# Kernel optimization log

Hardware: AMD Instinct MI355X
Metric: run time of the kernel (lower is better)

## Reference

```python
import jax, jax.numpy as jnp
import numpy as np

B, N_OBJ, N_VAL, E, H, HEADS = 512, 10, 200, 420, 128, 4
NPG = 1 + N_OBJ + N_VAL  # nodes per graph = 211
N = B * NPG
FMIN = float(np.finfo(np.float32).min)


def _gat_conv(x, src, dst, W, att_src, att_dst, bias, concat):
    # PyG GATConv (v1): linear (no bias) -> per-head attention logits ->
    # leaky_relu(a_src[j]+a_dst[i]) -> softmax over edges grouped by dst -> scatter-sum
    heads = att_src.shape[0]
    xs = (x @ W).reshape(N, heads, -1)            # [N, heads, C]
    a_src = (xs * att_src).sum(-1)                # [N, heads]
    a_dst = (xs * att_dst).sum(-1)                # [N, heads]
    alpha = jax.nn.leaky_relu(a_src[src] + a_dst[dst], 0.2)   # [Etot, heads]
    amax = jax.ops.segment_max(alpha, dst, num_segments=N)
    ex = jnp.exp(alpha - amax[dst])
    denom = jax.ops.segment_sum(ex, dst, num_segments=N)
    alpha = ex / (denom[dst] + 1e-16)
    out = jax.ops.segment_sum(xs[src] * alpha[..., None], dst, num_segments=N)  # [N,heads,C]
    out = out.reshape(N, -1) if concat else out.mean(axis=1)
    return out + bias


def setup_inputs() -> dict:
    key = jax.random.key(0)
    ks = jax.random.split(key, 24)
    s = 0.1
    C1 = H // HEADS  # 32
    inp = {
        'head_node': jax.random.normal(ks[0], (B, 2), jnp.float32),
        'objective_nodes': jax.random.normal(ks[1], (B, N_OBJ, 2), jnp.float32),
        'value_nodes': jax.random.normal(ks[2], (B, N_VAL, 5), jnp.float32),
        'edge_indices': jax.random.randint(ks[3], (B, 2, E), 0, NPG, jnp.int64 if jax.config.jax_enable_x64 else jnp.int32),
        'accept_mask': jnp.ones((B, 2), jnp.float32),
        'W_head': jax.random.normal(ks[4], (2, H)) * s, 'b_head': jnp.zeros((H,)),
        'W_obj': jax.random.normal(ks[5], (2, H)) * s, 'b_obj': jnp.zeros((H,)),
        'W_val': jax.random.normal(ks[6], (5, H)) * s, 'b_val': jnp.zeros((H,)),
        'W1': jax.random.normal(ks[7], (H, HEADS * C1)) * s,
        'att_src1': jax.random.normal(ks[8], (HEADS, C1)) * s,
        'att_dst1': jax.random.normal(ks[9], (HEADS, C1)) * s,
        'b1': jnp.zeros((HEADS * C1,)),
        'W2': jax.random.normal(ks[10], (H, HEADS * H)) * s,
        'att_src2': jax.random.normal(ks[11], (HEADS, H)) * s,
        'att_dst2': jax.random.normal(ks[12], (HEADS, H)) * s,
        'b2': jnp.zeros((H,)),
        'W_acc': jax.random.normal(ks[13], (H, 2)) * 0.01, 'b_acc': jnp.zeros((2,)),
        'W_off': jax.random.normal(ks[14], (H, 1)) * 0.01, 'b_off': jnp.zeros((1,)),
        'W_vf': jax.random.normal(ks[15], (H, 1)) * s, 'b_vf': jnp.zeros((1,)),
    }
    return inp


def reference(head_node, objective_nodes, value_nodes, edge_indices, accept_mask,
              W_head, b_head, W_obj, b_obj, W_val, b_val,
              W1, att_src1, att_dst1, b1, W2, att_src2, att_dst2, b2,
              W_acc, b_acc, W_off, b_off, W_vf, b_vf):
    # node encoders + ReLU
    h_head = jax.nn.relu(head_node @ W_head + b_head)                  # [B,H]
    h_obj = jax.nn.relu(objective_nodes @ W_obj + b_obj)               # [B,N_OBJ,H]
    h_val = jax.nn.relu(value_nodes @ W_val + b_val)                   # [B,N_VAL,H]
    h_nodes = jnp.concatenate([h_head[:, None], h_obj, h_val], axis=1)  # [B,NPG,H]
    x = h_nodes.reshape(N, H)
    # batch graphs: offset per-graph edge indices, add self loops
    offs = (jnp.arange(B, dtype=edge_indices.dtype) * NPG)[:, None, None]
    ei = (edge_indices + offs).transpose(1, 0, 2).reshape(2, -1)       # [2, B*E]
    loops = jnp.arange(N, dtype=edge_indices.dtype)
    src = jnp.concatenate([ei[0], loops])
    dst = jnp.concatenate([ei[1], loops])
    # GAT: layer1 concat heads, ReLU (BasicGNN inter-layer act), layer2 mean heads
    x1 = jax.nn.relu(_gat_conv(x, src, dst, W1, att_src1, att_dst1, b1, True))
    x2 = _gat_conv(x1, src, dst, W2, att_src2, att_dst2, b2, False)
    h_out = jax.nn.relu(x2).reshape(B, NPG, H)
    h_head_out = h_out[:, 0]                                           # [B,H]
    h_val_out = h_out[:, -N_VAL:]                                      # [B,N_VAL,H]
    offer_logits = (h_val_out @ W_off + b_off).squeeze(-1)             # [B,N_VAL]
    accept_inf_mask = jnp.maximum(jnp.log(accept_mask), FMIN)
    accept_logits = h_head_out @ W_acc + b_acc + accept_inf_mask       # [B,2]
    vf = h_head_out @ W_vf + b_vf                                      # [B,1]
    return jnp.concatenate([accept_logits, offer_logits, vf], axis=-1)  # [B, 2+N_VAL+1]
```

## Files before the change

kernel.cpp:

```cpp
#include <hip/hip_runtime.h>

typedef unsigned short u16;
typedef unsigned int u32;
typedef short short8 __attribute__((ext_vector_type(8)));
typedef float f32x4 __attribute__((ext_vector_type(4)));

#define NB   512
#define NPG  211
#define NOBJ 10
#define NVAL 200
#define NE   420
#define NN   (NB * NPG)

__device__ __forceinline__ float bf2f(u16 u){
  union { unsigned i; float f; } v; v.i = ((unsigned)u) << 16; return v.f;
}
__device__ __forceinline__ u16 f2bf(float f){
  union { float f; unsigned i; } v; v.f = f;
  return (u16)((v.i + 0x7FFFu + ((v.i >> 16) & 1u)) >> 16);
}
__device__ __forceinline__ float lo_bf(u32 u){ union{u32 i;float f;}v; v.i=u<<16; return v.f; }
__device__ __forceinline__ float hi_bf(u32 u){ union{u32 i;float f;}v; v.i=u&0xffff0000u; return v.f; }
__device__ __forceinline__ u32 pack_bf(float a, float b){ return (u32)f2bf(a) | ((u32)f2bf(b)<<16); }
__device__ __forceinline__ float lrelu(float s){ return s > 0.f ? s : 0.2f * s; }
__device__ __forceinline__ short8 pack8(ushort4 a, ushort4 b){
  short8 v;
  v[0]=(short)a.x; v[1]=(short)a.y; v[2]=(short)a.z; v[3]=(short)a.w;
  v[4]=(short)b.x; v[5]=(short)b.y; v[6]=(short)b.z; v[7]=(short)b.w;
  return v;
}
__device__ __forceinline__ int s16(int r, int c){
  return (r << 7) + ((((c >> 3) ^ (r & 15)) << 3) | (c & 7));
}

#define AS_GLOBAL(p) ((const __attribute__((address_space(1))) void*)((const void*)(p)))
#define AS_LDS(p)    ((__attribute__((address_space(3))) void*)((void*)(p)))

__global__ __launch_bounds__(256) void k_prep(const float* __restrict__ W1, const float* __restrict__ W2,
                                              const float* __restrict__ as2, const float* __restrict__ ad2,
                                              u16* __restrict__ W1t, u16* __restrict__ W2t,
                                              float* __restrict__ wms, float* __restrict__ wmd,
                                              u16* __restrict__ W2z){
  int gid = blockIdx.x * 256 + threadIdx.x;
  if (gid < 16384){
    int k = gid >> 7, n = gid & 127;
    W1t[n * 128 + k] = f2bf(W1[k * 128 + n]);
  } else if (gid < 81920){
    int t = gid - 16384;
    int n = t >> 9, kk = t & 511;
    int h = kk >> 7, c = kk & 127;
    W2t[n * 512 + kk] = f2bf(W2[c * 512 + h * 128 + n]);
  } else if (gid < 82944){
    int t = gid - 81920;
    int which = t >> 9, hk = t & 511;
    int h = hk >> 7, k = hk & 127;
    const float* av = which ? ad2 : as2;
    float s = 0.f;
    for (int j = 0; j < 128; ++j)
      s += W2[k * 512 + h * 128 + j] * av[h * 128 + j];
    (which ? wmd : wms)[hk] = s;
  } else {
    int t = gid - 82944;
    int c = t >> 7, k = t & 127;
    W2z[c * 128 + k] = f2bf(W2[k * 512 + c]);
  }
}

__global__ __launch_bounds__(256) void k_embed2(
    const float* __restrict__ head, const float* __restrict__ obj, const float* __restrict__ val,
    const float* __restrict__ Wh, const float* __restrict__ bh,
    const float* __restrict__ Wo, const float* __restrict__ bo,
    const float* __restrict__ Wv, const float* __restrict__ bv,
    u16* __restrict__ x){
  int gid = blockIdx.x * 256 + threadIdx.x;
  int n = gid >> 5, cc = (gid & 31) << 2;
  int g = n / NPG, loc = n - g * NPG;
  float a[4];
  if (loc == 0){
    const float* in = head + (size_t)g * 2;
    float i0 = in[0], i1 = in[1];
    #pragma unroll
    for (int t = 0; t < 4; ++t){ int c = cc + t; a[t] = bh[c] + i0 * Wh[c] + i1 * Wh[128 + c]; }
  } else if (loc <= NOBJ){
    const float* in = obj + ((size_t)g * NOBJ + (loc - 1)) * 2;
    float i0 = in[0], i1 = in[1];
    #pragma unroll
    for (int t = 0; t < 4; ++t){ int c = cc + t; a[t] = bo[c] + i0 * Wo[c] + i1 * Wo[128 + c]; }
  } else {
    const float* in = val + ((size_t)g * NVAL + (loc - 11)) * 5;
    float f[5];
    #pragma unroll
    for (int k = 0; k < 5; ++k) f[k] = in[k];
    #pragma unroll
    for (int t = 0; t < 4; ++t){
      int c = cc + t; float s = bv[c];
      #pragma unroll
      for (int k = 0; k < 5; ++k) s += f[k] * Wv[k * 128 + c];
      a[t] = s;
    }
  }
  ushort4 u;
  u.x = f2bf(fmaxf(a[0], 0.f)); u.y = f2bf(fmaxf(a[1], 0.f));
  u.z = f2bf(fmaxf(a[2], 0.f)); u.w = f2bf(fmaxf(a[3], 0.f));
  *(ushort4*)&x[(size_t)n * 128 + cc] = u;
}

__global__ __launch_bounds__(256) void k_csr2(const int* __restrict__ eidx,
                                              int* __restrict__ coff, int* __restrict__ csrc){
  __shared__ int sEs[420], sEd[420], sTmp[256], sOff[212], sSrc[632];
  int g = blockIdx.x, tid = threadIdx.x;
  const int4* e4 = (const int4*)(eidx + (size_t)g * 840);
  for (int i = tid; i < 105; i += 256){ ((int4*)sEs)[i] = e4[i]; ((int4*)sEd)[i] = e4[105 + i]; }
  __syncthreads();
  int deg = 0;
  if (tid < NPG){
    deg = 1;
    const int4* p4 = (const int4*)sEd;
    #pragma unroll 4
    for (int i = 0; i < 105; ++i){
      int4 v = p4[i];
      deg += (v.x == tid) + (v.y == tid) + (v.z == tid) + (v.w == tid);
    }
  }
  int v = deg;
  #pragma unroll
  for (int st = 1; st < 256; st <<= 1){
    sTmp[tid] = v;
    __syncthreads();
    if (tid >= st) v += sTmp[tid - st];
    __syncthreads();
  }
  if (tid < NPG) sOff[tid] = v - deg;
  if (tid == NPG - 1) sOff[NPG] = v;
  __syncthreads();
  if (tid < NPG){
    int p = sOff[tid];
    sSrc[p++] = tid;
    const int4* pd4 = (const int4*)sEd;
    const int4* ps4 = (const int4*)sEs;
    for (int i = 0; i < 105; ++i){
      int4 d = pd4[i]; int4 s = ps4[i];
      if (d.x == tid) sSrc[p++] = s.x;
      if (d.y == tid) sSrc[p++] = s.y;
      if (d.z == tid) sSrc[p++] = s.z;
      if (d.w == tid) sSrc[p++] = s.w;
    }
  }
  __syncthreads();
  if (tid < 212) coff[(size_t)g * 212 + tid] = sOff[tid];
  for (int i = tid; i < 631; i += 256) csrc[(size_t)g * 632 + i] = sSrc[i];
}

template<int KCH, bool RELU>
__global__ __launch_bounds__(512) void k_mm(const u16* __restrict__ A, int aStride, int chunkOff,
                                            const u16* __restrict__ Bt, int bstride,
                                            const float* __restrict__ bias, u16* __restrict__ C){
  __shared__ u16 sA[128 * 128];
  __shared__ u16 sB[128 * 128];
  const int tid = threadIdx.x, lane = tid & 63, w = tid >> 6;
  const int l15 = lane & 15, lg = lane >> 4;
  const int row0 = blockIdx.x * 128;
  f32x4 acc[8];
  #pragma unroll
  for (int ni = 0; ni < 8; ++ni) acc[ni] = (f32x4){0,0,0,0};

  #pragma unroll 1
  for (int ch = 0; ch < KCH; ++ch){
    const u16* Ab = A + (size_t)ch * chunkOff;
    const u16* Bb = Bt + ch * 128;
    #pragma unroll
    for (int i = 0; i < 4; ++i){
      int r = w * 16 + i * 4 + (lane >> 4);
      int c16 = lane & 15;
      int sw = (c16 ^ (r & 15)) << 4;
      __builtin_amdgcn_global_load_lds(AS_GLOBAL((const char*)(Ab + (size_t)(row0 + r) * aStride) + sw),
                                       AS_LDS(&sA[(w * 16 + i * 4) * 128]), 16, 0, 0);
      __builtin_amdgcn_global_load_lds(AS_GLOBAL((const char*)(Bb + (size_t)r * bstride) + sw),
                                       AS_LDS(&sB[(w * 16 + i * 4) * 128]), 16, 0, 0);
    }
    __syncthreads();
    #pragma unroll
    for (int kk = 0; kk < 4; ++kk){
      int k0 = kk * 32 + lg * 4;
      int rr = w * 16 + l15;
      short8 af = pack8(*(const ushort4*)&sA[s16(rr, k0)],
                        *(const ushort4*)&sA[s16(rr, k0 + 16)]);
      #pragma unroll
      for (int ni = 0; ni < 8; ++ni){
        int cc = ni * 16 + l15;
        short8 bf = pack8(*(const ushort4*)&sB[s16(cc, k0)],
                          *(const ushort4*)&sB[s16(cc, k0 + 16)]);
        acc[ni] = __builtin_amdgcn_mfma_f32_16x16x32_bf16(af, bf, acc[ni], 0, 0, 0);
      }
    }
    __syncthreads();
  }
  const int r0 = row0 + w * 16 + lg * 4;
  #pragma unroll
  for (int ni = 0; ni < 8; ++ni){
    int col = ni * 16 + l15;
    float bv = RELU ? bias[col] : 0.f;
    #pragma unroll
    for (int r = 0; r < 4; ++r){
      float v = acc[ni][r];
      if (RELU) v = fmaxf(v + bv, 0.f);
      C[(size_t)(r0 + r) * 128 + col] = f2bf(v);
    }
  }
}

__global__ __launch_bounds__(512) void k_mmz(const u16* __restrict__ A,
                                             const u16* __restrict__ W2z,
                                             u16* __restrict__ z){
  __shared__ u16 sA[128 * 128];
  __shared__ u16 sB[128 * 128];
  const int tid = threadIdx.x, lane = tid & 63, w = tid >> 6;
  const int l15 = lane & 15, lg = lane >> 4;
  const int row0 = (blockIdx.x >> 2) * 128;
  const int cy   = blockIdx.x & 3;
  const u16* Bb = W2z + cy * 16384;
  f32x4 acc[8];
  #pragma unroll
  for (int ni = 0; ni < 8; ++ni) acc[ni] = (f32x4){0,0,0,0};

  #pragma unroll
  for (int i = 0; i < 4; ++i){
    int r = w * 16 + i * 4 + (lane >> 4);
    int c16 = lane & 15;
    int sw = (c16 ^ (r & 15)) << 4;
    __builtin_amdgcn_global_load_lds(AS_GLOBAL((const char*)(A + (size_t)(row0 + r) * 128) + sw),
                                     AS_LDS(&sA[(w * 16 + i * 4) * 128]), 16, 0, 0);
    __builtin_amdgcn_global_load_lds(AS_GLOBAL((const char*)(Bb + (size_t)r * 128) + sw),
                                     AS_LDS(&sB[(w * 16 + i * 4) * 128]), 16, 0, 0);
  }
  __syncthreads();
  #pragma unroll
  for (int kk = 0; kk < 4; ++kk){
    int k0 = kk * 32 + lg * 4;
    int rr = w * 16 + l15;
    short8 af = pack8(*(const ushort4*)&sA[s16(rr, k0)],
                      *(const ushort4*)&sA[s16(rr, k0 + 16)]);
    #pragma unroll
    for (int ni = 0; ni < 8; ++ni){
      int cc = ni * 16 + l15;
      short8 bf = pack8(*(const ushort4*)&sB[s16(cc, k0)],
                        *(const ushort4*)&sB[s16(cc, k0 + 16)]);
      acc[ni] = __builtin_amdgcn_mfma_f32_16x16x32_bf16(af, bf, acc[ni], 0, 0, 0);
    }
  }
  const int r0 = row0 + w * 16 + lg * 4;
  #pragma unroll
  for (int ni = 0; ni < 8; ++ni){
    int col = cy * 128 + ni * 16 + l15;
    #pragma unroll
    for (int r = 0; r < 4; ++r)
      z[(size_t)(r0 + r) * 512 + col] = f2bf(acc[ni][r]);
  }
}

__global__ __launch_bounds__(512) void k_attsm1(const u16* __restrict__ xs1,
                                                const float* __restrict__ as1, const float* __restrict__ ad1,
                                                const int* __restrict__ coff, const int* __restrict__ csrc,
                                                float* __restrict__ wn, float* __restrict__ rden){
  __shared__ float sLs[844], sLd[844];
  const int g = blockIdx.x, tid = threadIdx.x;
  const int gb = g * NPG;
  for (int t = tid; t < NPG * 4; t += 512){
    int n = t >> 2, h = t & 3;
    const u16* xr = xs1 + (size_t)(gb + n) * 128 + h * 32;
    float s = 0.f, d = 0.f;
    #pragma unroll
    for (int j = 0; j < 8; ++j){
      ushort4 xv = *(const ushort4*)(xr + j * 4);
      #pragma unroll
      for (int q = 0; q < 4; ++q){
        float xf = bf2f(((const u16*)&xv)[q]);
        int c = h * 32 + j * 4 + q;
        s += xf * as1[c];
        d += xf * ad1[c];
      }
    }
    sLs[t] = s; sLd[t] = d;
  }
  __syncthreads();
  for (int t = tid; t < NPG * 4; t += 512){
    int dst = t >> 2, h = t & 3;
    int o0 = coff[(size_t)g * 212 + dst], o1 = coff[(size_t)g * 212 + dst + 1];
    const int* sp = csrc + (size_t)g * 632;
    float ad = sLd[t];
    float m = -3e38f;
    for (int e = o0; e < o1; ++e) m = fmaxf(m, lrelu(sLs[sp[e] * 4 + h] + ad));
    float dn = 0.f;
    float* wp = wn + (size_t)g * 2528 + h * 632;
    for (int e = o0; e < o1; ++e){
      float ee = __expf(lrelu(sLs[sp[e] * 4 + h] + ad) - m);
      wp[e] = ee; dn += ee;
    }
    rden[(size_t)(gb + dst) * 4 + h] = 1.0f / (dn + 1e-16f);
  }
}

__global__ __launch_bounds__(512) void k_attsm2(const u16* __restrict__ x1,
                                                const float* __restrict__ wms, const float* __restrict__ wmd,
                                                const int* __restrict__ coff, const int* __restrict__ csrc,
                                                float* __restrict__ wn, float* __restrict__ rden){
  __shared__ float sw[1024];
  __shared__ float sLs[844], sLd[844];
  const int g = blockIdx.x, tid = threadIdx.x;
  const int gb = g * NPG;
  for (int i = tid; i < 1024; i += 512) sw[i] = (i < 512) ? wms[i] : wmd[i - 512];
  __syncthreads();
  for (int t = tid; t < NPG * 4; t += 512){
    int n = t >> 2, h = t & 3;
    const u16* xr = x1 + (size_t)(gb + n) * 128;
    const float* wsp = sw + h * 128;
    const float* wdp = sw + 512 + h * 128;
    float s = 0.f, d = 0.f;
    #pragma unroll
    for (int j = 0; j < 32; ++j){
      ushort4 xv = *(const ushort4*)(xr + j * 4);
      #pragma unroll
      for (int q = 0; q < 4; ++q){
        float xf = bf2f(((const u16*)&xv)[q]);
        s += xf * wsp[j * 4 + q];
        d += xf * wdp[j * 4 + q];
      }
    }
    sLs[t] = s; sLd[t] = d;
  }
  __syncthreads();
  for (int t = tid; t < NPG * 4; t += 512){
    int dst = t >> 2, h = t & 3;
    int o0 = coff[(size_t)g * 212 + dst], o1 = coff[(size_t)g * 212 + dst + 1];
    const int* sp = csrc + (size_t)g * 632;
    float ad = sLd[t];
    float m = -3e38f;
    for (int e = o0; e < o1; ++e) m = fmaxf(m, lrelu(sLs[sp[e] * 4 + h] + ad));
    float dn = 0.f;
    float* wp = wn + (size_t)g * 2528 + h * 632;
    for (int e = o0; e < o1; ++e){
      float ee = __expf(lrelu(sLs[sp[e] * 4 + h] + ad) - m);
      wp[e] = ee; dn += ee;
    }
    rden[(size_t)(gb + dst) * 4 + h] = 0.25f / (dn + 1e-16f);
  }
}

__global__ __launch_bounds__(256) void k_gat1k(const u16* __restrict__ xs1,
                                               const float* __restrict__ wn, const float* __restrict__ rden,
                                               const int* __restrict__ coff, const int* __restrict__ csrc,
                                               const float* __restrict__ b1, u16* __restrict__ x1){
  int bid = blockIdx.x;
  int g = bid / 53, ch = bid - g * 53;
  int dst = ch * 4 + (threadIdx.x >> 6);
  if (dst >= NPG) return;
  int lane = threadIdx.x & 63;
  int cp = lane << 1, hh = lane >> 4;
  int gb = g * NPG;
  int o0 = coff[(size_t)g * 212 + dst], o1 = coff[(size_t)g * 212 + dst + 1];
  const int* sp = csrc + (size_t)g * 632;
  const float* wp = wn + (size_t)g * 2528 + hh * 632;
  float a0 = 0.f, a1 = 0.f;
  for (int e = o0; e < o1; ++e){
    int src = sp[e];
    u32 f = *(const u32*)&xs1[(size_t)(gb + src) * 128 + cp];
    float w = wp[e];
    a0 += w * lo_bf(f); a1 += w * hi_bf(f);
  }
  float rv = rden[(size_t)(gb + dst) * 4 + hh];
  *(u32*)&x1[(size_t)(gb + dst) * 128 + cp] =
    pack_bf(fmaxf(a0 * rv + b1[cp], 0.f), fmaxf(a1 * rv + b1[cp + 1], 0.f));
}

__global__ __launch_bounds__(256) void k_aggp(const u16* __restrict__ z,
                                              const float* __restrict__ wn, const float* __restrict__ rden,
                                              const int* __restrict__ coff, const int* __restrict__ csrc,
                                              const float* __restrict__ b2, const float* __restrict__ amask,
                                              const float* __restrict__ Wacc, const float* __restrict__ bacc,
                                              const float* __restrict__ Woff, const float* __restrict__ boff,
                                              const float* __restrict__ Wvf,  const float* __restrict__ bvf,
                                              float* __restrict__ out){
  int bid = blockIdx.x;
  int g = bid / 51, chunk = bid - g * 51;
  int idx = chunk * 4 + (threadIdx.x >> 6);
  if (idx >= 201) return;
  int dst = (idx == 0) ? 0 : 10 + idx;
  int lane = threadIdx.x & 63;
  int cp = lane << 1;
  int gb = g * NPG;
  int o0 = coff[(size_t)g * 212 + dst], o1 = coff[(size_t)g * 212 + dst + 1];
  const int* sp = csrc + (size_t)g * 632;
  const float* wb = wn + (size_t)g * 2528;
  float a00 = 0, a01 = 0, a10 = 0, a11 = 0, a20 = 0, a21 = 0, a30 = 0, a31 = 0;
  for (int e = o0; e < o1; ++e){
    int src = sp[e];
    const u16* zr = z + (size_t)(gb + src) * 512 + cp;
    u32 f0 = *(const u32*)&zr[0];
    u32 f1 = *(const u32*)&zr[128];
    u32 f2 = *(const u32*)&zr[256];
    u32 f3 = *(const u32*)&zr[384];
    float w0 = wb[e], w1 = wb[632 + e], w2 = wb[1264 + e], w3 = wb[1896 + e];
    a00 += w0 * lo_bf(f0); a01 += w0 * hi_bf(f0);
    a10 += w1 * lo_bf(f1); a11 += w1 * hi_bf(f1);
    a20 += w2 * lo_bf(f2); a21 += w2 * hi_bf(f2);
    a30 += w3 * lo_bf(f3); a31 += w3 * hi_bf(f3);
  }
  float4 rv = *(const float4*)&rden[(size_t)(gb + dst) * 4];
  float o2a = fmaxf(b2[cp]     + rv.x * a00 + rv.y * a10 + rv.z * a20 + rv.w * a30, 0.f);
  float o2b = fmaxf(b2[cp + 1] + rv.x * a01 + rv.y * a11 + rv.z * a21 + rv.w * a31, 0.f);
  if (idx == 0){
    float pA0 = o2a * Wacc[cp * 2]     + o2b * Wacc[(cp + 1) * 2];
    float pA1 = o2a * Wacc[cp * 2 + 1] + o2b * Wacc[(cp + 1) * 2 + 1];
    float pV  = o2a * Wvf[cp]          + o2b * Wvf[cp + 1];
    #pragma unroll
    for (int s = 1; s < 64; s <<= 1){
      pA0 += __shfl_xor(pA0, s);
      pA1 += __shfl_xor(pA1, s);
      pV  += __shfl_xor(pV, s);
    }
    if (lane == 0){
      float lm0 = fmaxf(logf(amask[g * 2]),     -3.402823466e38f);
      float lm1 = fmaxf(logf(amask[g * 2 + 1]), -3.402823466e38f);
      out[(size_t)g * 203]       = pA0 + bacc[0] + lm0;
      out[(size_t)g * 203 + 1]   = pA1 + bacc[1] + lm1;
      out[(size_t)g * 203 + 202] = pV + bvf[0];
    }
  } else {
    float pO = o2a * Woff[cp] + o2b * Woff[cp + 1];
    #pragma unroll
    for (int s = 1; s < 64; s <<= 1) pO += __shfl_xor(pO, s);
    if (lane == 0) out[(size_t)g * 203 + 2 + (idx - 1)] = pO + boff[0];
  }
}

extern "C" void kernel_launch(void* const* d_in, const int* in_sizes, int n_in,
                              void* d_out, int out_size, void* d_ws, size_t ws_size,
                              hipStream_t stream){
  (void)in_sizes; (void)n_in; (void)out_size; (void)ws_size;
  const float* head = (const float*)d_in[0];
  const float* obj  = (const float*)d_in[1];
  const float* val  = (const float*)d_in[2];
  const int*   eidx = (const int*)d_in[3];
  const float* amask= (const float*)d_in[4];
  const float* Wh   = (const float*)d_in[5];
  const float* bh   = (const float*)d_in[6];
  const float* Wo   = (const float*)d_in[7];
  const float* bo   = (const float*)d_in[8];
  const float* Wv   = (const float*)d_in[9];
  const float* bv   = (const float*)d_in[10];
  const float* W1   = (const float*)d_in[11];
  const float* as1  = (const float*)d_in[12];
  const float* ad1  = (const float*)d_in[13];
  const float* b1   = (const float*)d_in[14];
  const float* W2   = (const float*)d_in[15];
  const float* as2  = (const float*)d_in[16];
  const float* ad2  = (const float*)d_in[17];
  const float* b2   = (const float*)d_in[18];
  const float* Wacc = (const float*)d_in[19];
  const float* bacc = (const float*)d_in[20];
  const float* Woff = (const float*)d_in[21];
  const float* boff = (const float*)d_in[22];
  const float* Wvf  = (const float*)d_in[23];
  const float* bvf  = (const float*)d_in[24];
  float* out = (float*)d_out;

  char* ws = (char*)d_ws;
  u16*   W1t = (u16*)ws;
  u16*   W2t = (u16*)(ws + 32768);
  float* wms = (float*)(ws + 163840);
  float* wmd = (float*)(ws + 165888);
  int*   coff = (int*)(ws + 167936);
  int*   csrc = (int*)(ws + 602112);
  u16*   W2z  = (u16*)(ws + 1896448);
  float* wn   = (float*)(ws + 5353472);
  float* rden = (float*)(ws + 10530816);
  u16*   x    = (u16*)(ws + 12259328);
  u16*   xs1  = (u16*)(ws + 39915520);
  u16*   z    = (u16*)(ws + 67571712);

  k_prep<<<580, 256, 0, stream>>>(W1, W2, as2, ad2, W1t, W2t, wms, wmd, W2z);
  k_embed2<<<NN * 32 / 256, 256, 0, stream>>>(head, obj, val, Wh, bh, Wo, bo, Wv, bv, x);
  k_csr2<<<NB, 256, 0, stream>>>(eidx, coff, csrc);
  k_mm<1, false><<<NN / 128, 512, 0, stream>>>(x, 128, 0, W1t, 128, nullptr, xs1);
  k_attsm1<<<NB, 512, 0, stream>>>(xs1, as1, ad1, coff, csrc, wn, rden);
  k_gat1k<<<NB * 53, 256, 0, stream>>>(xs1, wn, rden, coff, csrc, b1, x);
  k_attsm2<<<NB, 512, 0, stream>>>(x, wms, wmd, coff, csrc, wn, rden);
  k_mmz<<<(NN / 128) * 4, 512, 0, stream>>>(x, W2z, z);
  k_aggp<<<NB * 51, 256, 0, stream>>>(z, wn, rden, coff, csrc, b2, amask,
                                      Wacc, bacc, Woff, boff, Wvf, bvf, out);
}
```

Baseline: 253.8 us.

## Fuse layer-2 aggregation before projection into one kernel with output heads

Reorders GAT layer 2 to aggregate the 128-wide layer-1 features per head first, then multiply by W2 with MFMA, using linearity. This replaces the separate z=x1@W2 matmul, which wrote a 512-wide intermediate, and the gather kernel that read it back. The new fused kernel computes attention-weighted aggregates into LDS, accumulates across heads in MFMA, and applies bias, ReLU and the output projections in place. It also remaps blocks to XCDs so neighbouring row tiles land together. In exchange it now computes all nodes, including objective nodes whose output is discarded, and the per-row serial gather runs inside the matmul block, which may limit overlap.

Measured after the change: 329.2 us. 1.3x slower.

```diff
diff --git a/kernel.cpp b/kernel.cpp
--- a/kernel.cpp
+++ b/kernel.cpp
@@ -39,8 +39,7 @@
 __global__ __launch_bounds__(256) void k_prep(const float* __restrict__ W1, const float* __restrict__ W2,
                                               const float* __restrict__ as2, const float* __restrict__ ad2,
                                               u16* __restrict__ W1t, u16* __restrict__ W2t,
-                                              float* __restrict__ wms, float* __restrict__ wmd,
-                                              u16* __restrict__ W2z){
+                                              float* __restrict__ wms, float* __restrict__ wmd){
   int gid = blockIdx.x * 256 + threadIdx.x;
   if (gid < 16384){
     int k = gid >> 7, n = gid & 127;
@@ -50,7 +49,7 @@
     int n = t >> 9, kk = t & 511;
     int h = kk >> 7, c = kk & 127;
     W2t[n * 512 + kk] = f2bf(W2[c * 512 + h * 128 + n]);
-  } else if (gid < 82944){
+  } else {
     int t = gid - 81920;
     int which = t >> 9, hk = t & 511;
     int h = hk >> 7, k = hk & 127;
@@ -59,10 +58,6 @@
     for (int j = 0; j < 128; ++j)
       s += W2[k * 512 + h * 128 + j] * av[h * 128 + j];
     (which ? wmd : wms)[hk] = s;
-  } else {
-    int t = gid - 82944;
-    int c = t >> 7, k = t & 127;
-    W2z[c * 128 + k] = f2bf(W2[k * 512 + c]);
   }
 }
 
@@ -206,55 +201,6 @@
       if (RELU) v = fmaxf(v + bv, 0.f);
       C[(size_t)(r0 + r) * 128 + col] = f2bf(v);
     }
-  }
-}
-
-__global__ __launch_bounds__(512) void k_mmz(const u16* __restrict__ A,
-                                             const u16* __restrict__ W2z,
-                                             u16* __restrict__ z){
-  __shared__ u16 sA[128 * 128];
-  __shared__ u16 sB[128 * 128];
-  const int tid = threadIdx.x, lane = tid & 63, w = tid >> 6;
-  const int l15 = lane & 15, lg = lane >> 4;
-  const int row0 = (blockIdx.x >> 2) * 128;
-  const int cy   = blockIdx.x & 3;
-  const u16* Bb = W2z + cy * 16384;
-  f32x4 acc[8];
-  #pragma unroll
-  for (int ni = 0; ni < 8; ++ni) acc[ni] = (f32x4){0,0,0,0};
-
-  #pragma unroll
-  for (int i = 0; i < 4; ++i){
-    int r = w * 16 + i * 4 + (lane >> 4);
-    int c16 = lane & 15;
-    int sw = (c16 ^ (r & 15)) << 4;
-    __builtin_amdgcn_global_load_lds(AS_GLOBAL((const char*)(A + (size_t)(row0 + r) * 128) + sw),
-                                     AS_LDS(&sA[(w * 16 + i * 4) * 128]), 16, 0, 0);
-    __builtin_amdgcn_global_load_lds(AS_GLOBAL((const char*)(Bb + (size_t)r * 128) + sw),
-                                     AS_LDS(&sB[(w * 16 + i * 4) * 128]), 16, 0, 0);
-  }
-  __syncthreads();
-  #pragma unroll
-  for (int kk = 0; kk < 4; ++kk){
-    int k0 = kk * 32 + lg * 4;
-    int rr = w * 16 + l15;
-    short8 af = pack8(*(const ushort4*)&sA[s16(rr, k0)],
-                      *(const ushort4*)&sA[s16(rr, k0 + 16)]);
-    #pragma unroll
-    for (int ni = 0; ni < 8; ++ni){
-      int cc = ni * 16 + l15;
-      short8 bf = pack8(*(const ushort4*)&sB[s16(cc, k0)],
-                        *(const ushort4*)&sB[s16(cc, k0 + 16)]);
-      acc[ni] = __builtin_amdgcn_mfma_f32_16x16x32_bf16(af, bf, acc[ni], 0, 0, 0);
-    }
-  }
-  const int r0 = row0 + w * 16 + lg * 4;
-  #pragma unroll
-  for (int ni = 0; ni < 8; ++ni){
-    int col = cy * 128 + ni * 16 + l15;
-    #pragma unroll
-    for (int r = 0; r < 4; ++r)
-      z[(size_t)(r0 + r) * 512 + col] = f2bf(acc[ni][r]);
   }
 }
 
@@ -372,64 +318,127 @@
     pack_bf(fmaxf(a0 * rv + b1[cp], 0.f), fmaxf(a1 * rv + b1[cp + 1], 0.f));
 }
 
-__global__ __launch_bounds__(256) void k_aggp(const u16* __restrict__ z,
-                                              const float* __restrict__ wn, const float* __restrict__ rden,
-                                              const int* __restrict__ coff, const int* __restrict__ csrc,
-                                              const float* __restrict__ b2, const float* __restrict__ amask,
-                                              const float* __restrict__ Wacc, const float* __restrict__ bacc,
-                                              const float* __restrict__ Woff, const float* __restrict__ boff,
-                                              const float* __restrict__ Wvf,  const float* __restrict__ bvf,
-                                              float* __restrict__ out){
-  int bid = blockIdx.x;
-  int g = bid / 51, chunk = bid - g * 51;
-  int idx = chunk * 4 + (threadIdx.x >> 6);
-  if (idx >= 201) return;
-  int dst = (idx == 0) ? 0 : 10 + idx;
-  int lane = threadIdx.x & 63;
-  int cp = lane << 1;
-  int gb = g * NPG;
-  int o0 = coff[(size_t)g * 212 + dst], o1 = coff[(size_t)g * 212 + dst + 1];
-  const int* sp = csrc + (size_t)g * 632;
-  const float* wb = wn + (size_t)g * 2528;
-  float a00 = 0, a01 = 0, a10 = 0, a11 = 0, a20 = 0, a21 = 0, a30 = 0, a31 = 0;
-  for (int e = o0; e < o1; ++e){
-    int src = sp[e];
-    const u16* zr = z + (size_t)(gb + src) * 512 + cp;
-    u32 f0 = *(const u32*)&zr[0];
-    u32 f1 = *(const u32*)&zr[128];
-    u32 f2 = *(const u32*)&zr[256];
-    u32 f3 = *(const u32*)&zr[384];
-    float w0 = wb[e], w1 = wb[632 + e], w2 = wb[1264 + e], w3 = wb[1896 + e];
-    a00 += w0 * lo_bf(f0); a01 += w0 * hi_bf(f0);
-    a10 += w1 * lo_bf(f1); a11 += w1 * hi_bf(f1);
-    a20 += w2 * lo_bf(f2); a21 += w2 * hi_bf(f2);
-    a30 += w3 * lo_bf(f3); a31 += w3 * hi_bf(f3);
-  }
-  float4 rv = *(const float4*)&rden[(size_t)(gb + dst) * 4];
-  float o2a = fmaxf(b2[cp]     + rv.x * a00 + rv.y * a10 + rv.z * a20 + rv.w * a30, 0.f);
-  float o2b = fmaxf(b2[cp + 1] + rv.x * a01 + rv.y * a11 + rv.z * a21 + rv.w * a31, 0.f);
-  if (idx == 0){
-    float pA0 = o2a * Wacc[cp * 2]     + o2b * Wacc[(cp + 1) * 2];
-    float pA1 = o2a * Wacc[cp * 2 + 1] + o2b * Wacc[(cp + 1) * 2 + 1];
-    float pV  = o2a * Wvf[cp]          + o2b * Wvf[cp + 1];
-    #pragma unroll
-    for (int s = 1; s < 64; s <<= 1){
-      pA0 += __shfl_xor(pA0, s);
-      pA1 += __shfl_xor(pA1, s);
-      pV  += __shfl_xor(pV, s);
-    }
-    if (lane == 0){
-      float lm0 = fmaxf(logf(amask[g * 2]),     -3.402823466e38f);
-      float lm1 = fmaxf(logf(amask[g * 2 + 1]), -3.402823466e38f);
-      out[(size_t)g * 203]       = pA0 + bacc[0] + lm0;
-      out[(size_t)g * 203 + 1]   = pA1 + bacc[1] + lm1;
-      out[(size_t)g * 203 + 202] = pV + bvf[0];
-    }
-  } else {
-    float pO = o2a * Woff[cp] + o2b * Woff[cp + 1];
-    #pragma unroll
-    for (int s = 1; s < 64; s <<= 1) pO += __shfl_xor(pO, s);
-    if (lane == 0) out[(size_t)g * 203 + 2 + (idx - 1)] = pO + boff[0];
+__global__ __launch_bounds__(512) void k_yagg(
+    const u16* __restrict__ x1, const float* __restrict__ wn, const float* __restrict__ rden,
+    const int* __restrict__ coff, const int* __restrict__ csrc,
+    const u16* __restrict__ W2t, const float* __restrict__ b2,
+    const float* __restrict__ amask,
+    const float* __restrict__ Wacc, const float* __restrict__ bacc,
+    const float* __restrict__ Woff, const float* __restrict__ boff,
+    const float* __restrict__ Wvf,  const float* __restrict__ bvf,
+    float* __restrict__ out)
+{
+  __shared__ u16 sA[128 * 128];
+  __shared__ u16 sB[128 * 128];
+  const int tid = threadIdx.x, lane = tid & 63, w = tid >> 6;
+  const int l15 = lane & 15, lg = lane >> 4;
+  const int cp = lane << 1;
+  const int xcd = blockIdx.x & 7, j = blockIdx.x >> 3;
+  const int nb  = (xcd < 4 ? xcd * 106 : 4 * 106 + (xcd - 4) * 105) + j;
+  const int row0 = nb * 128;
+
+  f32x4 acc[8];
+  #pragma unroll
+  for (int ni = 0; ni < 8; ++ni) acc[ni] = (f32x4){0,0,0,0};
+
+  #pragma unroll 1
+  for (int h = 0; h < 4; ++h){
+    #pragma unroll
+    for (int i = 0; i < 4; ++i){
+      int r = w * 16 + i * 4 + (lane >> 4);
+      int c16 = lane & 15;
+      int sw = (c16 ^ (r & 15)) << 4;
+      __builtin_amdgcn_global_load_lds(AS_GLOBAL((const char*)(W2t + (size_t)r * 512 + h * 128) + sw),
+                                       AS_LDS(&sB[(w * 16 + i * 4) * 128]), 16, 0, 0);
+    }
+    for (int t = 0; t < 16; ++t){
+      int row = row0 + w * 16 + t;
+      int g = row / NPG, loc = row - g * NPG;
+      int gb = g * NPG;
+      int o0 = coff[(size_t)g * 212 + loc], o1 = coff[(size_t)g * 212 + loc + 1];
+      const int* sp = csrc + (size_t)g * 632;
+      const float* wp = wn + (size_t)g * 2528 + h * 632;
+      float a0 = 0.f, a1 = 0.f;
+      int e = o0;
+      for (; e + 4 <= o1; e += 4){
+        int s0 = sp[e], s1 = sp[e+1], s2 = sp[e+2], s3 = sp[e+3];
+        u32 f0 = *(const u32*)&x1[(size_t)(gb + s0) * 128 + cp];
+        u32 f1 = *(const u32*)&x1[(size_t)(gb + s1) * 128 + cp];
+        u32 f2 = *(const u32*)&x1[(size_t)(gb + s2) * 128 + cp];
+        u32 f3 = *(const u32*)&x1[(size_t)(gb + s3) * 128 + cp];
+        float w0 = wp[e], w1 = wp[e+1], w2 = wp[e+2], w3 = wp[e+3];
+        a0 += w0 * lo_bf(f0); a1 += w0 * hi_bf(f0);
+        a0 += w1 * lo_bf(f1); a1 += w1 * hi_bf(f1);
+        a0 += w2 * lo_bf(f2); a1 += w2 * hi_bf(f2);
+        a0 += w3 * lo_bf(f3); a1 += w3 * hi_bf(f3);
+      }
+      for (; e < o1; ++e){
+        int src = sp[e];
+        u32 f = *(const u32*)&x1[(size_t)(gb + src) * 128 + cp];
+        float wv = wp[e];
+        a0 += wv * lo_bf(f); a1 += wv * hi_bf(f);
+      }
+      float rv = rden[(size_t)row * 4 + h];
+      *(u32*)&sA[s16(w * 16 + t, cp)] = pack_bf(a0 * rv, a1 * rv);
+    }
+    __syncthreads();
+    #pragma unroll
+    for (int kk = 0; kk < 4; ++kk){
+      int k0 = kk * 32 + lg * 4;
+      int rr = w * 16 + l15;
+      short8 af = pack8(*(const ushort4*)&sA[s16(rr, k0)],
+                        *(const ushort4*)&sA[s16(rr, k0 + 16)]);
+      #pragma unroll
+      for (int ni = 0; ni < 8; ++ni){
+        int cc = ni * 16 + l15;
+        short8 bf = pack8(*(const ushort4*)&sB[s16(cc, k0)],
+                          *(const ushort4*)&sB[s16(cc, k0 + 16)]);
+        acc[ni] = __builtin_amdgcn_mfma_f32_16x16x32_bf16(af, bf, acc[ni], 0, 0, 0);
+      }
+    }
+    __syncthreads();
+  }
+
+  float bv[8];
+  #pragma unroll
+  for (int ni = 0; ni < 8; ++ni) bv[ni] = b2[ni * 16 + l15];
+  #pragma unroll
+  for (int r = 0; r < 4; ++r){
+    int row = row0 + w * 16 + lg * 4 + r;
+    int g = row / NPG, loc = row - g * NPG;
+    float v[8];
+    #pragma unroll
+    for (int ni = 0; ni < 8; ++ni) v[ni] = fmaxf(acc[ni][r] + bv[ni], 0.f);
+    if (loc == 0){
+      float pA0 = 0.f, pA1 = 0.f, pV = 0.f;
+      #pragma unroll
+      for (int ni = 0; ni < 8; ++ni){
+        int c = ni * 16 + l15;
+        pA0 += v[ni] * Wacc[c * 2];
+        pA1 += v[ni] * Wacc[c * 2 + 1];
+        pV  += v[ni] * Wvf[c];
+      }
+      #pragma unroll
+      for (int s = 1; s < 16; s <<= 1){
+        pA0 += __shfl_xor(pA0, s);
+        pA1 += __shfl_xor(pA1, s);
+        pV  += __shfl_xor(pV, s);
+      }
+      if (l15 == 0){
+        float lm0 = fmaxf(logf(amask[g * 2]),     -3.402823466e38f);
+        float lm1 = fmaxf(logf(amask[g * 2 + 1]), -3.402823466e38f);
+        out[(size_t)g * 203]       = pA0 + bacc[0] + lm0;
+        out[(size_t)g * 203 + 1]   = pA1 + bacc[1] + lm1;
+        out[(size_t)g * 203 + 202] = pV + bvf[0];
+      }
+    } else if (loc >= 11){
+      float pO = 0.f;
+      #pragma unroll
+      for (int ni = 0; ni < 8; ++ni) pO += v[ni] * Woff[ni * 16 + l15];
+      #pragma unroll
+      for (int s = 1; s < 16; s <<= 1) pO += __shfl_xor(pO, s);
+      if (l15 == 0) out[(size_t)g * 203 + 2 + (loc - 11)] = pO + boff[0];
+    }
   }
 }
 
@@ -471,21 +480,18 @@
   float* wmd = (float*)(ws + 165888);
   int*   coff = (int*)(ws + 167936);
   int*   csrc = (int*)(ws + 602112);
-  u16*   W2z  = (u16*)(ws + 1896448);
   float* wn   = (float*)(ws + 5353472);
   float* rden = (float*)(ws + 10530816);
   u16*   x    = (u16*)(ws + 12259328);
   u16*   xs1  = (u16*)(ws + 39915520);
-  u16*   z    = (u16*)(ws + 67571712);
-
-  k_prep<<<580, 256, 0, stream>>>(W1, W2, as2, ad2, W1t, W2t, wms, wmd, W2z);
+
+  k_prep<<<324, 256, 0, stream>>>(W1, W2, as2, ad2, W1t, W2t, wms, wmd);
   k_embed2<<<NN * 32 / 256, 256, 0, stream>>>(head, obj, val, Wh, bh, Wo, bo, Wv, bv, x);
   k_csr2<<<NB, 256, 0, stream>>>(eidx, coff, csrc);
   k_mm<1, false><<<NN / 128, 512, 0, stream>>>(x, 128, 0, W1t, 128, nullptr, xs1);
   k_attsm1<<<NB, 512, 0, stream>>>(xs1, as1, ad1, coff, csrc, wn, rden);
   k_gat1k<<<NB * 53, 256, 0, stream>>>(xs1, wn, rden, coff, csrc, b1, x);
   k_attsm2<<<NB, 512, 0, stream>>>(x, wms, wmd, coff, csrc, wn, rden);
-  k_mmz<<<(NN / 128) * 4, 512, 0, stream>>>(x, W2z, z);
-  k_aggp<<<NB * 51, 256, 0, stream>>>(z, wn, rden, coff, csrc, b2, amask,
-                                      Wacc, bacc, Woff, boff, Wvf, bvf, out);
-}
+  k_yagg<<<NN / 128, 512, 0, stream>>>(x, wn, rden, coff, csrc, W2t, b2, amask,
+                                       Wacc, bacc, Woff, boff, Wvf, bvf, out);
+}
```
